# Kernel tuning notes

Hardware: AMD Instinct MI355X
Metric: run time of the kernel (lower is better)

The kernel has to match this reference:

```python
import jax, jax.numpy as jnp
import numpy as np

DIM = 768
NUM_HEADS = 12
POLY_DEG = 3
GRID = (24, 24)
BATCH = 16


def _make_powers():
    H, W = GRID
    ii, jj = np.meshgrid(np.arange(H), np.arange(W), indexing='ij')
    coords = np.stack([ii.ravel(), jj.ravel()], axis=-1).astype(np.float32)  # [HW, 2]
    dists = np.abs(coords[:, None, :] - coords[None, :, :]).sum(-1)  # L1 cdist [HW, HW]
    powers = np.stack([dists ** i for i in range(POLY_DEG + 1)], axis=0)  # [deg+1, HW, HW]
    return jnp.asarray(powers, dtype=jnp.float32)


def setup_inputs() -> dict:
    key = jax.random.key(0)
    ks = jax.random.split(key, 5)
    N = GRID[0] * GRID[1] + 1  # 577
    x = jax.random.normal(ks[0], (BATCH, N, DIM), dtype=jnp.float32)
    # nn.Linear weights stored as [in, out] for direct matmul; qkv_bias=False
    W_qkv = jax.random.normal(ks[1], (DIM, 3 * DIM), dtype=jnp.float32) * (DIM ** -0.5)
    W_proj = jax.random.normal(ks[2], (DIM, DIM), dtype=jnp.float32) * (DIM ** -0.5)
    b_proj = jnp.zeros((DIM,), dtype=jnp.float32)
    # small scale keeps polynomial bias (distances up to 46, cubed) numerically sane
    poly_coeffs = jax.random.normal(ks[3], (NUM_HEADS, POLY_DEG + 1), dtype=jnp.float32) * 0.01
    powers = _make_powers()
    return {"x": x, "W_qkv": W_qkv, "W_proj": W_proj, "b_proj": b_proj,
            "poly_coeffs": poly_coeffs, "powers": powers}


def reference(x, W_qkv, W_proj, b_proj, poly_coeffs, powers):
    B, N, C = x.shape
    h = NUM_HEADS
    d = C // h
    scale = d ** -0.5
    qkv = (x @ W_qkv).reshape(B, N, 3, h, d)
    qkv = jnp.transpose(qkv, (2, 0, 3, 1, 4))  # [3, B, h, N, d]
    q, k, v = qkv[0], qkv[1], qkv[2]
    # polynomial relative-position bias, padded with zeros for CLS row/col
    rpe = jnp.einsum('hd,dxy->hxy', poly_coeffs, powers)  # [h, HW, HW]
    rpe = jnp.pad(rpe, ((0, 0), (1, 0), (1, 0)))  # [h, N, N]
    attn = scale * jnp.einsum('bhnd,bhmd->bhnm', q, k) + rpe[None]
    attn = jax.nn.softmax(attn, axis=-1)
    out = jnp.einsum('bhnm,bhmd->bhnd', attn, v)
    out = jnp.transpose(out, (0, 2, 1, 3)).reshape(B, N, C)
    return out @ W_proj + b_proj
```

## Files before the change

### kernel.cpp

```cpp
#include <hip/hip_runtime.h>


using u16 = unsigned short;
using u32 = unsigned int;

typedef __bf16 bf16x8 __attribute__((ext_vector_type(8)));
typedef float f32x4 __attribute__((ext_vector_type(4)));

__device__ inline u16 f2bf(float f) {
    u32 u = __builtin_bit_cast(u32, f);
    u32 r = u + 0x7fffu + ((u >> 16) & 1u);
    return (u16)(r >> 16);
}
__device__ inline float bf2f(u16 x) {
    return __builtin_bit_cast(float, (u32)x << 16);
}

__device__ inline f32x4 mfma16(bf16x8 a, bf16x8 b, f32x4 c) {
    return __builtin_amdgcn_mfma_f32_16x16x32_bf16(a, b, c, 0, 0, 0);
}

__device__ inline float fexp2(float x) { return __builtin_amdgcn_exp2f(x); }

__device__ inline int xcd_remap(int bid, int nwg) {
    const int q = nwg >> 3, r = nwg & 7;
    const int xcd = bid & 7, idx = bid >> 3;
    return (xcd < r ? xcd * (q + 1) : r * (q + 1) + (xcd - r) * q) + idx;
}

__device__ inline float dpp_max16(float v) {
    int x;
    x = __builtin_amdgcn_update_dpp(0, __builtin_bit_cast(int, v), 0xB1, 0xF, 0xF, true);
    v = fmaxf(v, __builtin_bit_cast(float, x));
    x = __builtin_amdgcn_update_dpp(0, __builtin_bit_cast(int, v), 0x4E, 0xF, 0xF, true);
    v = fmaxf(v, __builtin_bit_cast(float, x));
    x = __builtin_amdgcn_update_dpp(0, __builtin_bit_cast(int, v), 0x124, 0xF, 0xF, true);
    v = fmaxf(v, __builtin_bit_cast(float, x));
    x = __builtin_amdgcn_update_dpp(0, __builtin_bit_cast(int, v), 0x128, 0xF, 0xF, true);
    v = fmaxf(v, __builtin_bit_cast(float, x));
    return v;
}
__device__ inline float dpp_sum16(float v) {
    int x;
    x = __builtin_amdgcn_update_dpp(0, __builtin_bit_cast(int, v), 0xB1, 0xF, 0xF, true);
    v += __builtin_bit_cast(float, x);
    x = __builtin_amdgcn_update_dpp(0, __builtin_bit_cast(int, v), 0x4E, 0xF, 0xF, true);
    v += __builtin_bit_cast(float, x);
    x = __builtin_amdgcn_update_dpp(0, __builtin_bit_cast(int, v), 0x124, 0xF, 0xF, true);
    v += __builtin_bit_cast(float, x);
    x = __builtin_amdgcn_update_dpp(0, __builtin_bit_cast(int, v), 0x128, 0xF, 0xF, true);
    v += __builtin_bit_cast(float, x);
    return v;
}

#define GLOAD_LDS16(g, l)                                                          \
    __builtin_amdgcn_global_load_lds((const __attribute__((address_space(1))) u32*)(g), \
                                     (__attribute__((address_space(3))) u32*)(l), 16, 0, 0)

#define BAR()    asm volatile("s_barrier" ::: "memory")
#define WAITV8() asm volatile("s_waitcnt vmcnt(8)" ::: "memory")
#define WAITV4() asm volatile("s_waitcnt vmcnt(4)" ::: "memory")
#define WAITV0() asm volatile("s_waitcnt vmcnt(0)" ::: "memory")

__global__ void k_prep(const float* __restrict__ x, const float* __restrict__ Wq,
                       const float* __restrict__ Wp, u16* __restrict__ xb,
                       u16* __restrict__ wqkv, u16* __restrict__ wprj) {
    const int bid = blockIdx.x;
    const int t = threadIdx.x;
    if (bid < 576) {
        __shared__ float tile[64][65];
        const float* src;
        u16* dst;
        int C, rt, ct;
        if (bid < 432) { src = Wq; dst = wqkv; C = 2304; rt = bid / 36; ct = bid % 36; }
        else { const int b2 = bid - 432; src = Wp; dst = wprj; C = 768; rt = b2 / 12; ct = b2 % 12; }
        const int row0 = rt * 64, col0 = ct * 64;
#pragma unroll
        for (int it = 0; it < 4; ++it) {
            const int row = it * 16 + (t >> 4);
            const float4 v = *(const float4*)&src[(size_t)(row0 + row) * C + col0 + (t & 15) * 4];
            tile[row][(t & 15) * 4 + 0] = v.x;
            tile[row][(t & 15) * 4 + 1] = v.y;
            tile[row][(t & 15) * 4 + 2] = v.z;
            tile[row][(t & 15) * 4 + 3] = v.w;
        }
        __syncthreads();
#pragma unroll
        for (int it = 0; it < 4; ++it) {
            const int oc = it * 16 + (t >> 4);
            const int orr = (t & 15) * 4;
            ushort4 o;
            o.x = f2bf(tile[orr + 0][oc]);
            o.y = f2bf(tile[orr + 1][oc]);
            o.z = f2bf(tile[orr + 2][oc]);
            o.w = f2bf(tile[orr + 3][oc]);
            *(ushort4*)&dst[(size_t)(col0 + oc) * 768 + row0 + orr] = o;
        }
    } else {
        const int n4 = 9232 * 768 / 4;
        const int stride = (2048 - 576) * 256;
        for (int i = (bid - 576) * 256 + t; i < n4; i += stride) {
            float4 v = ((const float4*)x)[i];
            ushort4 o;
            o.x = f2bf(v.x); o.y = f2bf(v.y); o.z = f2bf(v.z); o.w = f2bf(v.w);
            ((ushort4*)xb)[i] = o;
        }
    }
}

__device__ inline void stageAB(const u16* __restrict__ Ag, const u16* __restrict__ Bg,
                               u16* L, int t) {
#pragma unroll
    for (int c = 0; c < 2; ++c) {
        const int p = c * 256 + t;
        const int row = p >> 2, ch = p & 3;
        const int src = row * 768 + ((ch ^ ((row >> 1) & 3)) * 8);
        GLOAD_LDS16(Ag + src, L + p * 8);
        GLOAD_LDS16(Bg + src, L + 4096 + p * 8);
    }
}
__device__ inline bf16x8 ldfrag32(const u16* base, int row, int slot) {
    return *(const bf16x8*)(base + row * 32 + ((slot ^ ((row >> 1) & 3)) * 8));
}

template <int MODE, int NB>
__launch_bounds__(256, 2)
__global__ void k_gemm(const u16* __restrict__ A, const u16* __restrict__ Bw,
                       u16* __restrict__ q_out, u16* __restrict__ k_out,
                       u16* __restrict__ v_out,
                       float* __restrict__ f_out, const float* __restrict__ bias) {
    constexpr int NT = 24;
    constexpr int M = 9232;
    const int wgid = xcd_remap(blockIdx.x, gridDim.x);
    const int mbase = (wgid / NB) * 128;
    const int nbase = (wgid - (wgid / NB) * NB) * 128;
    __shared__ alignas(16) u16 lds[4][8192];
    const int t = threadIdx.x;
    const int lane = t & 63, w = t >> 6;
    const int lr = lane & 15, lg = lane >> 4;
    const int wrow = (w >> 1) * 64, wcol = (w & 1) * 64;
    const u16* Ag = A + (size_t)mbase * 768;
    const u16* Bg = Bw + (size_t)nbase * 768;
    f32x4 acc[4][4] = {};

    stageAB(Ag, Bg, &lds[0][0], t);
    stageAB(Ag + 32, Bg + 32, &lds[1][0], t);
    stageAB(Ag + 64, Bg + 64, &lds[2][0], t);
    WAITV8();
    BAR();

    for (int kt = 0; kt < NT; ++kt) {
        const u16* Lc = &lds[kt & 3][0];
        if (kt + 3 < NT)
            stageAB(Ag + (kt + 3) * 32, Bg + (kt + 3) * 32, &lds[(kt + 3) & 3][0], t);
        bf16x8 af[4], bv[4];
#pragma unroll
        for (int i = 0; i < 4; ++i)
            af[i] = ldfrag32(Lc, wrow + i * 16 + lr, lg);
#pragma unroll
        for (int j = 0; j < 4; ++j)
            bv[j] = ldfrag32(Lc + 4096, wcol + j * 16 + lr, lg);
        __builtin_amdgcn_s_setprio(1);
#pragma unroll
        for (int i = 0; i < 4; ++i)
#pragma unroll
            for (int j = 0; j < 4; ++j)
                acc[i][j] = mfma16(af[i], bv[j], acc[i][j]);
        __builtin_amdgcn_s_setprio(0);
        if (kt + 1 < NT) {
            if (kt < NT - 3)       { WAITV8(); }
            else if (kt == NT - 3) { WAITV4(); }
            else                   { WAITV0(); }
            BAR();
        }
    }

#pragma unroll
    for (int i = 0; i < 4; ++i) {
#pragma unroll
        for (int j = 0; j < 4; ++j) {
            const int col = nbase + wcol + j * 16 + lr;
#pragma unroll
            for (int r = 0; r < 4; ++r) {
                const int row = mbase + wrow + i * 16 + 4 * lg + r;
                if (row < M) {
                    if (MODE == 0) {
                        const int bb = row / 577;
                        const int nn = row - bb * 577;
                        const int tt = col / 768;
                        const int rem = col - tt * 768;
                        const int hh = rem >> 6, dd = rem & 63;
                        const size_t bh = (size_t)bb * 12 + hh;
                        const u16 val = f2bf(acc[i][j][r]);
                        if (tt == 0)      q_out[(bh * 640 + nn) * 64 + dd] = val;
                        else if (tt == 1) k_out[(bh * 640 + nn) * 64 + dd] = val;
                        else              v_out[(bh * 64 + dd) * 640 + nn] = val;
                    } else {
                        f_out[(size_t)row * 768 + col] = acc[i][j][r] + bias[col];
                    }
                }
            }
        }
    }
}

__launch_bounds__(256, 4)
__global__ void k_attn(const u16* __restrict__ Qg, const u16* __restrict__ Kg,
                       const u16* __restrict__ Vtg, const float* __restrict__ coef,
                       u16* __restrict__ Og) {
    const int wgid = xcd_remap(blockIdx.x, gridDim.x);
    const int bh = wgid / 9;
    const int qt = wgid - bh * 9;
    const int b = bh / 12, h = bh - b * 12;
    const int t = threadIdx.x;
    const int lane = t & 63, w = t >> 6;
    const int lr = lane & 15, lg = lane >> 4;
    __shared__ alignas(16) u16 Kl[2][4096];
    __shared__ alignas(16) u16 Vl[2][4096];
    __shared__ float lut[48];

    {
        const float l2e = 1.4426950408889634f;
        const float c0 = coef[h * 4 + 0] * l2e, c1 = coef[h * 4 + 1] * l2e,
                    c2 = coef[h * 4 + 2] * l2e, c3 = coef[h * 4 + 3] * l2e;
        if (t < 48) {
            const float d = (float)t;
            lut[t] = (t <= 46) ? (((c3 * d + c2) * d + c1) * d + c0) : 0.f;
        }
    }

    const int qrow0 = qt * 64 + w * 16;
    const u16* qp = Qg + ((size_t)bh * 640 + qrow0 + lr) * 64;
    const bf16x8 qa0 = *(const bf16x8*)(qp + lg * 8);
    const bf16x8 qa1 = *(const bf16x8*)(qp + 32 + lg * 8);

    float gi[4], gj[4];
#pragma unroll
    for (int r = 0; r < 4; ++r) {
        const int n = qrow0 + 4 * lg + r;
        if (n == 0) { gi[r] = 100.f; gj[r] = 0.f; }
        else {
            const int nm1 = n - 1;
            const int qi = nm1 / 24;
            gi[r] = (float)qi;
            gj[r] = (float)(nm1 - qi * 24);
        }
    }

    float M[4], L[4];
#pragma unroll
    for (int r = 0; r < 4; ++r) { M[r] = -3e38f; L[r] = 0.f; }
    f32x4 acco[4] = {};
    const float scale2 = 0.125f * 1.4426950408889634f;
    const int ch0 = ((lg ^ (lr & 7))) * 8;

    const u16* Ksb = Kg + (size_t)bh * 640 * 64;
    const u16* Vsb = Vtg + (size_t)bh * 64 * 640;
    const int pr0 = t >> 3, pc0 = t & 7;
    const int pr1 = (256 + t) >> 3, pc1 = (256 + t) & 7;
    const int kd0 = pr0 * 64 + ((pc0 ^ (pr0 & 7)) * 8);
    const int kd1 = pr1 * 64 + ((pc1 ^ (pr1 & 7)) * 8);
    const int vr0 = 16 * w + (lane >> 3), vc = lane & 7;
    const int vr1 = vr0 + 8;
    const int vd0 = vr0 * 64 + ((vc ^ (vr0 & 7)) * 8);
    const int vd1 = vr1 * 64 + ((vc ^ (vr1 & 7)) * 8);

    {
        uint4 k0 = *(const uint4*)(Ksb + pr0 * 64 + pc0 * 8);
        uint4 k1 = *(const uint4*)(Ksb + pr1 * 64 + pc1 * 8);
        uint4 v0 = *(const uint4*)(Vsb + (size_t)vr0 * 640 + vc * 8);
        uint4 v1 = *(const uint4*)(Vsb + (size_t)vr1 * 640 + vc * 8);
        *(uint4*)(&Kl[0][kd0]) = k0;
        *(uint4*)(&Kl[0][kd1]) = k1;
        *(uint4*)(&Vl[0][vd0]) = v0;
        *(uint4*)(&Vl[0][vd1]) = v1;
    }
    __syncthreads();
    int cur = 0;

    for (int kt = 0; kt < 9; ++kt) {
        const u16* Ks = Ksb + (size_t)(kt + 1) * 64 * 64;
        const u16* Vs = Vsb + (size_t)(kt + 1) * 64;
        const uint4 nk0 = *(const uint4*)(Ks + pr0 * 64 + pc0 * 8);
        const uint4 nk1 = *(const uint4*)(Ks + pr1 * 64 + pc1 * 8);
        const uint4 nv0 = *(const uint4*)(Vs + (size_t)vr0 * 640 + vc * 8);
        const uint4 nv1 = *(const uint4*)(Vs + (size_t)vr1 * 640 + vc * 8);

        const u16* Kc = &Kl[cur][0];
        const u16* Vc = &Vl[cur][0];
        u16* pw = &Vl[cur ^ 1][w * 1024];

        f32x4 sac[4];
        __builtin_amdgcn_s_setprio(1);
#pragma unroll
        for (int cb = 0; cb < 4; ++cb) {
            const int row = cb * 16 + lr;
            const bf16x8 kb0 = *(const bf16x8*)(Kc + row * 64 + ch0);
            const bf16x8 kb1 = *(const bf16x8*)(Kc + row * 64 + (ch0 ^ 32));
            f32x4 z = {};
            z = mfma16(qa0, kb0, z);
            sac[cb] = mfma16(qa1, kb1, z);
        }
        __builtin_amdgcn_s_setprio(0);

        float s[4][4], tm[4];
#pragma unroll
        for (int r = 0; r < 4; ++r) tm[r] = -3e38f;
#pragma unroll
        for (int cb = 0; cb < 4; ++cb) {
            const int m = kt * 64 + cb * 16 + lr;
            float ci, cj;
            if (m == 0) { ci = 200.f; cj = 0.f; }
            else {
                const int mm1 = m - 1;
                const int pi = mm1 / 24;
                ci = (float)pi;
                cj = (float)(mm1 - pi * 24);
            }
#pragma unroll
            for (int r = 0; r < 4; ++r) {
                const float df = fabsf(gi[r] - ci) + fabsf(gj[r] - cj);
                const int idx = min((int)df, 47);
                const float v = fmaf(sac[cb][r], scale2, lut[idx]);
                s[cb][r] = v;
                tm[r] = fmaxf(tm[r], v);
            }
        }
#pragma unroll
        for (int r = 0; r < 4; ++r) tm[r] = dpp_max16(tm[r]);

        float over = tm[0] - M[0];
        over = fmaxf(over, tm[1] - M[1]);
        over = fmaxf(over, tm[2] - M[2]);
        over = fmaxf(over, tm[3] - M[3]);
        if (__any(over > 11.5f)) {
#pragma unroll
            for (int r = 0; r < 4; ++r) {
                const float Mn = fmaxf(M[r], tm[r]);
                const float a = fexp2(M[r] - Mn);
                L[r] *= a;
                acco[0][r] *= a; acco[1][r] *= a;
                acco[2][r] *= a; acco[3][r] *= a;
                M[r] = Mn;
            }
        }

#pragma unroll
        for (int cb = 0; cb < 4; ++cb)
#pragma unroll
            for (int r = 0; r < 4; ++r) {
                const float p = fexp2(s[cb][r] - M[r]);
                L[r] += p;
                const int rw = 4 * lg + r;
                pw[rw * 64 + (((2 * cb + (lr >> 3)) ^ (rw & 7)) * 8) + (lr & 7)] = f2bf(p);
            }
        const bf16x8 pa0 = *(const bf16x8*)(pw + lr * 64 + ch0);
        const bf16x8 pa1 = *(const bf16x8*)(pw + lr * 64 + (ch0 ^ 32));
        __builtin_amdgcn_s_setprio(1);
#pragma unroll
        for (int f = 0; f < 4; ++f) {
            const int vrow = f * 16 + lr;
            const bf16x8 vb0 = *(const bf16x8*)(Vc + vrow * 64 + ch0);
            const bf16x8 vb1 = *(const bf16x8*)(Vc + vrow * 64 + (ch0 ^ 32));
            acco[f] = mfma16(pa0, vb0, acco[f]);
            acco[f] = mfma16(pa1, vb1, acco[f]);
        }
        __builtin_amdgcn_s_setprio(0);

        *(uint4*)(&Kl[cur ^ 1][kd0]) = nk0;
        *(uint4*)(&Kl[cur ^ 1][kd1]) = nk1;
        *(uint4*)(&Vl[cur ^ 1][vd0]) = nv0;
        *(uint4*)(&Vl[cur ^ 1][vd1]) = nv1;
        __syncthreads();
        cur ^= 1;
    }

    {
        const u16* Kc = &Kl[cur][0];
        const u16* Vc = &Vl[cur][0];
        u16* pw = &Vl[cur ^ 1][w * 1024];
        const bf16x8 kb0 = *(const bf16x8*)(Kc + lr * 64 + ch0);
        const bf16x8 kb1 = *(const bf16x8*)(Kc + lr * 64 + (ch0 ^ 32));
        f32x4 z = {};
        z = mfma16(qa0, kb0, z);
        const f32x4 sac0 = mfma16(qa1, kb1, z);

        float s0[4], tm[4];
#pragma unroll
        for (int r = 0; r < 4; ++r) {
            const float df = fabsf(gi[r] - 23.f) + fabsf(gj[r] - 23.f);
            float v = fmaf(sac0[r], scale2, lut[min((int)df, 47)]);
            v = (lr == 0) ? v : -1e30f;
            s0[r] = v;
            tm[r] = dpp_max16(v);
        }
        float over = tm[0] - M[0];
        over = fmaxf(over, tm[1] - M[1]);
        over = fmaxf(over, tm[2] - M[2]);
        over = fmaxf(over, tm[3] - M[3]);
        if (__any(over > 11.5f)) {
#pragma unroll
            for (int r = 0; r < 4; ++r) {
                const float Mn = fmaxf(M[r], tm[r]);
                const float a = fexp2(M[r] - Mn);
                L[r] *= a;
                acco[0][r] *= a; acco[1][r] *= a;
                acco[2][r] *= a; acco[3][r] *= a;
                M[r] = Mn;
            }
        }
#pragma unroll
        for (int cb = 0; cb < 4; ++cb)
#pragma unroll
            for (int r = 0; r < 4; ++r) {
                const float p = (cb == 0) ? fexp2(s0[r] - M[r]) : 0.f;
                L[r] += p;
                const int rw = 4 * lg + r;
                pw[rw * 64 + (((2 * cb + (lr >> 3)) ^ (rw & 7)) * 8) + (lr & 7)] = f2bf(p);
            }
        const bf16x8 pa0 = *(const bf16x8*)(pw + lr * 64 + ch0);
#pragma unroll
        for (int f = 0; f < 4; ++f) {
            const int vrow = f * 16 + lr;
            const bf16x8 vb0 = *(const bf16x8*)(Vc + vrow * 64 + ch0);
            acco[f] = mfma16(pa0, vb0, acco[f]);
        }
    }

    float inv[4];
#pragma unroll
    for (int r = 0; r < 4; ++r) inv[r] = __builtin_amdgcn_rcpf(dpp_sum16(L[r]));
#pragma unroll
    for (int f = 0; f < 4; ++f)
#pragma unroll
        for (int r = 0; r < 4; ++r) {
            const int n = qrow0 + 4 * lg + r;
            Og[((size_t)b * 577 + n) * 768 + h * 64 + f * 16 + lr] =
                f2bf(acco[f][r] * inv[r]);
        }
}

__launch_bounds__(256)
__global__ void k_attn_last(const u16* __restrict__ Qg, const u16* __restrict__ Kg,
                            const u16* __restrict__ Vtg, const float* __restrict__ coef,
                            u16* __restrict__ Og) {
    const int bh = blockIdx.x;
    const int b = bh / 12, h = bh - b * 12;
    const int t = threadIdx.x;
    const int lane = t & 63, w = t >> 6;
    __shared__ float qs[64];
    __shared__ float ps[640];
    __shared__ float red[4];
    __shared__ float opart[4][64];
    const float l2e = 1.4426950408889634f;
    const float c0 = coef[h * 4 + 0] * l2e, c1 = coef[h * 4 + 1] * l2e,
                c2 = coef[h * 4 + 2] * l2e, c3 = coef[h * 4 + 3] * l2e;
    const float scale2 = 0.125f * l2e;

    if (t < 64) qs[t] = bf2f(Qg[((size_t)bh * 640 + 576) * 64 + t]);
    __syncthreads();

    float sv[3];
#pragma unroll
    for (int u = 0; u < 3; ++u) {
        const int k = t + u * 256;
        float s = -3e38f;
        if (k < 577) {
            const u16* kp = Kg + ((size_t)bh * 640 + k) * 64;
            float acc = 0.f;
            for (int j = 0; j < 64; ++j) acc += qs[j] * bf2f(kp[j]);
            float rv = 0.f;
            if (k >= 1) {
                const int km1 = k - 1;
                const int ki = km1 / 24;
                const float d = fabsf(23.f - (float)ki) + fabsf(23.f - (float)(km1 - ki * 24));
                rv = ((c3 * d + c2) * d + c1) * d + c0;
            }
            s = fmaf(acc, scale2, rv);
        }
        sv[u] = s;
    }
    float v = fmaxf(fmaxf(sv[0], sv[1]), sv[2]);
    v = fmaxf(v, __shfl_xor(v, 1));  v = fmaxf(v, __shfl_xor(v, 2));
    v = fmaxf(v, __shfl_xor(v, 4));  v = fmaxf(v, __shfl_xor(v, 8));
    v = fmaxf(v, __shfl_xor(v, 16)); v = fmaxf(v, __shfl_xor(v, 32));
    if (lane == 0) red[w] = v;
    __syncthreads();
    const float Mx = fmaxf(fmaxf(red[0], red[1]), fmaxf(red[2], red[3]));

    float lsum = 0.f;
#pragma unroll
    for (int u = 0; u < 3; ++u) {
        const int k = t + u * 256;
        const float p = (k < 577) ? fexp2(sv[u] - Mx) : 0.f;
        if (k < 640) ps[k] = p;
        lsum += p;
    }
    lsum += __shfl_xor(lsum, 1);  lsum += __shfl_xor(lsum, 2);
    lsum += __shfl_xor(lsum, 4);  lsum += __shfl_xor(lsum, 8);
    lsum += __shfl_xor(lsum, 16); lsum += __shfl_xor(lsum, 32);
    __syncthreads();
    if (lane == 0) red[w] = lsum;
    __syncthreads();
    const float Lx = red[0] + red[1] + red[2] + red[3];

    const int d = t & 63, qd = t >> 6;
    const u16* vp = Vtg + ((size_t)bh * 64 + d) * 640;
    float o = 0.f;
    for (int k = qd * 160; k < qd * 160 + 160; ++k) o += ps[k] * bf2f(vp[k]);
    opart[qd][d] = o;
    __syncthreads();
    if (t < 64) {
        const float oo = (opart[0][t] + opart[1][t] + opart[2][t] + opart[3][t]) / Lx;
        Og[((size_t)b * 577 + 576) * 768 + h * 64 + t] = f2bf(oo);
    }
}

extern "C" void kernel_launch(void* const* d_in, const int* in_sizes, int n_in,
                              void* d_out, int out_size, void* d_ws, size_t ws_size,
                              hipStream_t stream) {
    const float* x      = (const float*)d_in[0];
    const float* W_qkv  = (const float*)d_in[1];
    const float* W_proj = (const float*)d_in[2];
    const float* b_proj = (const float*)d_in[3];
    const float* coef   = (const float*)d_in[4];
    float* out = (float*)d_out;
    char* ws = (char*)d_ws;

    u16* xb   = (u16*)(ws + 0);
    u16* Og   = (u16*)(ws + 0);
    u16* wqkv = (u16*)(ws + 14180352);
    u16* wprj = (u16*)(ws + 17719296);
    u16* Qg   = (u16*)(ws + 18898944);
    u16* Kg   = (u16*)(ws + 34627584);
    u16* Vtg  = (u16*)(ws + 50356224);

    k_prep<<<2048, 256, 0, stream>>>(x, W_qkv, W_proj, xb, wqkv, wprj);

    k_gemm<0, 18><<<18 * 73, 256, 0, stream>>>(xb, wqkv, Qg, Kg, Vtg,
                                               nullptr, nullptr);
    k_attn<<<1728, 256, 0, stream>>>(Qg, Kg, Vtg, coef, Og);
    k_attn_last<<<192, 256, 0, stream>>>(Qg, Kg, Vtg, coef, Og);
    k_gemm<1, 6><<<6 * 73, 256, 0, stream>>>(Og, wprj, nullptr, nullptr,
                                             nullptr, out, b_proj);
}
```

Before: 171.9 us.

## Load GEMM fragments directly from global memory instead of LDS pipeline

Removes the 4-stage LDS staging buffer, the async global-to-LDS copies and the per-iteration barriers from the GEMM kernel. Each wave now loads its MFMA operand fragments straight from global memory, and the occupancy hint rises to 4 blocks per CU now that no LDS is used. This drops barrier and LDS traffic overhead but loses operand sharing between waves, duplicating global and L2 reads. There is also no explicit prefetch, so load latency must be hidden by occupancy.

Result: slower. 285.6 us (+66.2%).

```diff
diff --git a/kernel.cpp b/kernel.cpp
--- a/kernel.cpp
+++ b/kernel.cpp
@@ -52,15 +52,6 @@
     v += __builtin_bit_cast(float, x);
     return v;
 }
-
-#define GLOAD_LDS16(g, l)                                                          \
-    __builtin_amdgcn_global_load_lds((const __attribute__((address_space(1))) u32*)(g), \
-                                     (__attribute__((address_space(3))) u32*)(l), 16, 0, 0)
-
-#define BAR()    asm volatile("s_barrier" ::: "memory")
-#define WAITV8() asm volatile("s_waitcnt vmcnt(8)" ::: "memory")
-#define WAITV4() asm volatile("s_waitcnt vmcnt(4)" ::: "memory")
-#define WAITV0() asm volatile("s_waitcnt vmcnt(0)" ::: "memory")
 
 __global__ void k_prep(const float* __restrict__ x, const float* __restrict__ Wq,
                        const float* __restrict__ Wp, u16* __restrict__ xb,
@@ -108,23 +99,8 @@
     }
 }
 
-__device__ inline void stageAB(const u16* __restrict__ Ag, const u16* __restrict__ Bg,
-                               u16* L, int t) {
-#pragma unroll
-    for (int c = 0; c < 2; ++c) {
-        const int p = c * 256 + t;
-        const int row = p >> 2, ch = p & 3;
-        const int src = row * 768 + ((ch ^ ((row >> 1) & 3)) * 8);
-        GLOAD_LDS16(Ag + src, L + p * 8);
-        GLOAD_LDS16(Bg + src, L + 4096 + p * 8);
-    }
-}
-__device__ inline bf16x8 ldfrag32(const u16* base, int row, int slot) {
-    return *(const bf16x8*)(base + row * 32 + ((slot ^ ((row >> 1) & 3)) * 8));
-}
-
 template <int MODE, int NB>
-__launch_bounds__(256, 2)
+__launch_bounds__(256, 4)
 __global__ void k_gemm(const u16* __restrict__ A, const u16* __restrict__ Bw,
                        u16* __restrict__ q_out, u16* __restrict__ k_out,
                        u16* __restrict__ v_out,
@@ -134,32 +110,24 @@
     const int wgid = xcd_remap(blockIdx.x, gridDim.x);
     const int mbase = (wgid / NB) * 128;
     const int nbase = (wgid - (wgid / NB) * NB) * 128;
-    __shared__ alignas(16) u16 lds[4][8192];
     const int t = threadIdx.x;
     const int lane = t & 63, w = t >> 6;
     const int lr = lane & 15, lg = lane >> 4;
     const int wrow = (w >> 1) * 64, wcol = (w & 1) * 64;
-    const u16* Ag = A + (size_t)mbase * 768;
-    const u16* Bg = Bw + (size_t)nbase * 768;
+    const u16* Ap = A + (size_t)(mbase + wrow + lr) * 768 + lg * 8;
+    const u16* Bp = Bw + (size_t)(nbase + wcol + lr) * 768 + lg * 8;
     f32x4 acc[4][4] = {};
 
-    stageAB(Ag, Bg, &lds[0][0], t);
-    stageAB(Ag + 32, Bg + 32, &lds[1][0], t);
-    stageAB(Ag + 64, Bg + 64, &lds[2][0], t);
-    WAITV8();
-    BAR();
-
+#pragma unroll 1
     for (int kt = 0; kt < NT; ++kt) {
-        const u16* Lc = &lds[kt & 3][0];
-        if (kt + 3 < NT)
-            stageAB(Ag + (kt + 3) * 32, Bg + (kt + 3) * 32, &lds[(kt + 3) & 3][0], t);
+        const int ko = kt * 32;
         bf16x8 af[4], bv[4];
 #pragma unroll
         for (int i = 0; i < 4; ++i)
-            af[i] = ldfrag32(Lc, wrow + i * 16 + lr, lg);
+            af[i] = *(const bf16x8*)(Ap + i * (16 * 768) + ko);
 #pragma unroll
         for (int j = 0; j < 4; ++j)
-            bv[j] = ldfrag32(Lc + 4096, wcol + j * 16 + lr, lg);
+            bv[j] = *(const bf16x8*)(Bp + j * (16 * 768) + ko);
         __builtin_amdgcn_s_setprio(1);
 #pragma unroll
         for (int i = 0; i < 4; ++i)
@@ -167,12 +135,6 @@
             for (int j = 0; j < 4; ++j)
                 acc[i][j] = mfma16(af[i], bv[j], acc[i][j]);
         __builtin_amdgcn_s_setprio(0);
-        if (kt + 1 < NT) {
-            if (kt < NT - 3)       { WAITV8(); }
-            else if (kt == NT - 3) { WAITV4(); }
-            else                   { WAITV0(); }
-            BAR();
-        }
     }
 
 #pragma unroll
```

## Process 32 query rows per wave and fold last-row kernel into attention

Applied to the files above, without the earlier changes.

Each wave now handles two 16-row query tiles (128 rows per block, 5 tiles per head), so every K/V tile loaded into LDS feeds twice as many MFMAs. The separate scalar k_attn_last kernel for row 576 is removed because the 640-row padded tiling now covers it, with a guard on the output store. The P staging buffers are moved into the idle halves of the K and V double buffers, and the next-tile global loads are issued later in the loop. Costs are roughly doubled accumulator and score registers, possible occupancy loss under launch_bounds(256,4), fewer blocks (960 instead of 1728), and wasted work on padded rows.

New measurement: 217.9 us. 1.27x slower.

```diff
diff --git a/kernel.cpp b/kernel.cpp
--- a/kernel.cpp
+++ b/kernel.cpp
@@ -209,8 +209,8 @@
                        const u16* __restrict__ Vtg, const float* __restrict__ coef,
                        u16* __restrict__ Og) {
     const int wgid = xcd_remap(blockIdx.x, gridDim.x);
-    const int bh = wgid / 9;
-    const int qt = wgid - bh * 9;
+    const int bh = wgid / 5;
+    const int qt = wgid - bh * 5;
     const int b = bh / 12, h = bh - b * 12;
     const int t = threadIdx.x;
     const int lane = t & 63, w = t >> 6;
@@ -229,83 +229,86 @@
         }
     }
 
-    const int qrow0 = qt * 64 + w * 16;
-    const u16* qp = Qg + ((size_t)bh * 640 + qrow0 + lr) * 64;
-    const bf16x8 qa0 = *(const bf16x8*)(qp + lg * 8);
-    const bf16x8 qa1 = *(const bf16x8*)(qp + 32 + lg * 8);
-
-    float gi[4], gj[4];
-#pragma unroll
-    for (int r = 0; r < 4; ++r) {
-        const int n = qrow0 + 4 * lg + r;
-        if (n == 0) { gi[r] = 100.f; gj[r] = 0.f; }
-        else {
-            const int nm1 = n - 1;
-            const int qi = nm1 / 24;
-            gi[r] = (float)qi;
-            gj[r] = (float)(nm1 - qi * 24);
-        }
-    }
-
-    float M[4], L[4];
-#pragma unroll
-    for (int r = 0; r < 4; ++r) { M[r] = -3e38f; L[r] = 0.f; }
-    f32x4 acco[4] = {};
+    const int qrow0 = qt * 128 + w * 32;
+    bf16x8 qa[2][2];
+#pragma unroll
+    for (int i = 0; i < 2; ++i) {
+        const u16* qp = Qg + ((size_t)bh * 640 + qrow0 + i * 16 + lr) * 64;
+        qa[i][0] = *(const bf16x8*)(qp + lg * 8);
+        qa[i][1] = *(const bf16x8*)(qp + 32 + lg * 8);
+    }
+
+    float gi[2][4], gj[2][4];
+#pragma unroll
+    for (int i = 0; i < 2; ++i)
+#pragma unroll
+        for (int r = 0; r < 4; ++r) {
+            const int n = qrow0 + i * 16 + 4 * lg + r;
+            if (n == 0) { gi[i][r] = 100.f; gj[i][r] = 0.f; }
+            else {
+                const int nm1 = n - 1;
+                const int qi = nm1 / 24;
+                gi[i][r] = (float)qi;
+                gj[i][r] = (float)(nm1 - qi * 24);
+            }
+        }
+
+    float M[2][4], L[2][4];
+#pragma unroll
+    for (int i = 0; i < 2; ++i)
+#pragma unroll
+        for (int r = 0; r < 4; ++r) { M[i][r] = -3e38f; L[i][r] = 0.f; }
+    f32x4 acco[2][4] = {};
     const float scale2 = 0.125f * 1.4426950408889634f;
     const int ch0 = ((lg ^ (lr & 7))) * 8;
 
     const u16* Ksb = Kg + (size_t)bh * 640 * 64;
     const u16* Vsb = Vtg + (size_t)bh * 64 * 640;
-    const int pr0 = t >> 3, pc0 = t & 7;
-    const int pr1 = (256 + t) >> 3, pc1 = (256 + t) & 7;
-    const int kd0 = pr0 * 64 + ((pc0 ^ (pr0 & 7)) * 8);
-    const int kd1 = pr1 * 64 + ((pc1 ^ (pr1 & 7)) * 8);
-    const int vr0 = 16 * w + (lane >> 3), vc = lane & 7;
-    const int vr1 = vr0 + 8;
-    const int vd0 = vr0 * 64 + ((vc ^ (vr0 & 7)) * 8);
-    const int vd1 = vr1 * 64 + ((vc ^ (vr1 & 7)) * 8);
+    const int sr0 = lane >> 3, sc = lane & 7;
+    const int kr0 = 16 * w + sr0, kr1 = kr0 + 8;
+    const int kd0 = kr0 * 64 + ((sc ^ (kr0 & 7)) * 8);
+    const int kd1 = kr1 * 64 + ((sc ^ (kr1 & 7)) * 8);
 
     {
-        uint4 k0 = *(const uint4*)(Ksb + pr0 * 64 + pc0 * 8);
-        uint4 k1 = *(const uint4*)(Ksb + pr1 * 64 + pc1 * 8);
-        uint4 v0 = *(const uint4*)(Vsb + (size_t)vr0 * 640 + vc * 8);
-        uint4 v1 = *(const uint4*)(Vsb + (size_t)vr1 * 640 + vc * 8);
+        uint4 k0 = *(const uint4*)(Ksb + kr0 * 64 + sc * 8);
+        uint4 k1 = *(const uint4*)(Ksb + kr1 * 64 + sc * 8);
+        uint4 v0 = *(const uint4*)(Vsb + (size_t)kr0 * 640 + sc * 8);
+        uint4 v1 = *(const uint4*)(Vsb + (size_t)kr1 * 640 + sc * 8);
         *(uint4*)(&Kl[0][kd0]) = k0;
         *(uint4*)(&Kl[0][kd1]) = k1;
-        *(uint4*)(&Vl[0][vd0]) = v0;
-        *(uint4*)(&Vl[0][vd1]) = v1;
+        *(uint4*)(&Vl[0][kd0]) = v0;
+        *(uint4*)(&Vl[0][kd1]) = v1;
     }
     __syncthreads();
     int cur = 0;
 
     for (int kt = 0; kt < 9; ++kt) {
-        const u16* Ks = Ksb + (size_t)(kt + 1) * 64 * 64;
-        const u16* Vs = Vsb + (size_t)(kt + 1) * 64;
-        const uint4 nk0 = *(const uint4*)(Ks + pr0 * 64 + pc0 * 8);
-        const uint4 nk1 = *(const uint4*)(Ks + pr1 * 64 + pc1 * 8);
-        const uint4 nv0 = *(const uint4*)(Vs + (size_t)vr0 * 640 + vc * 8);
-        const uint4 nv1 = *(const uint4*)(Vs + (size_t)vr1 * 640 + vc * 8);
-
         const u16* Kc = &Kl[cur][0];
         const u16* Vc = &Vl[cur][0];
-        u16* pw = &Vl[cur ^ 1][w * 1024];
-
-        f32x4 sac[4];
+        u16* pb0 = &Kl[cur ^ 1][16 * w * 64];
+        u16* pb1 = &Vl[cur ^ 1][16 * w * 64];
+
+        f32x4 sac[2][4];
         __builtin_amdgcn_s_setprio(1);
 #pragma unroll
         for (int cb = 0; cb < 4; ++cb) {
             const int row = cb * 16 + lr;
             const bf16x8 kb0 = *(const bf16x8*)(Kc + row * 64 + ch0);
             const bf16x8 kb1 = *(const bf16x8*)(Kc + row * 64 + (ch0 ^ 32));
-            f32x4 z = {};
-            z = mfma16(qa0, kb0, z);
-            sac[cb] = mfma16(qa1, kb1, z);
+#pragma unroll
+            for (int i = 0; i < 2; ++i) {
+                f32x4 z = {};
+                z = mfma16(qa[i][0], kb0, z);
+                sac[i][cb] = mfma16(qa[i][1], kb1, z);
+            }
         }
         __builtin_amdgcn_s_setprio(0);
 
-        float s[4][4], tm[4];
-#pragma unroll
-        for (int r = 0; r < 4; ++r) tm[r] = -3e38f;
+        float tm[2][4];
+#pragma unroll
+        for (int i = 0; i < 2; ++i)
+#pragma unroll
+            for (int r = 0; r < 4; ++r) tm[i][r] = -3e38f;
 #pragma unroll
         for (int cb = 0; cb < 4; ++cb) {
             const int m = kt * 64 + cb * 16 + lr;
@@ -318,59 +321,84 @@
                 cj = (float)(mm1 - pi * 24);
             }
 #pragma unroll
-            for (int r = 0; r < 4; ++r) {
-                const float df = fabsf(gi[r] - ci) + fabsf(gj[r] - cj);
-                const int idx = min((int)df, 47);
-                const float v = fmaf(sac[cb][r], scale2, lut[idx]);
-                s[cb][r] = v;
-                tm[r] = fmaxf(tm[r], v);
-            }
-        }
-#pragma unroll
-        for (int r = 0; r < 4; ++r) tm[r] = dpp_max16(tm[r]);
-
-        float over = tm[0] - M[0];
-        over = fmaxf(over, tm[1] - M[1]);
-        over = fmaxf(over, tm[2] - M[2]);
-        over = fmaxf(over, tm[3] - M[3]);
+            for (int i = 0; i < 2; ++i)
+#pragma unroll
+                for (int r = 0; r < 4; ++r) {
+                    const float df = fabsf(gi[i][r] - ci) + fabsf(gj[i][r] - cj);
+                    const float v = fmaf(sac[i][cb][r], scale2, lut[min((int)df, 47)]);
+                    sac[i][cb][r] = v;
+                    tm[i][r] = fmaxf(tm[i][r], v);
+                }
+        }
+#pragma unroll
+        for (int i = 0; i < 2; ++i)
+#pragma unroll
+            for (int r = 0; r < 4; ++r) tm[i][r] = dpp_max16(tm[i][r]);
+
+        float over = -3e38f;
+#pragma unroll
+        for (int i = 0; i < 2; ++i)
+#pragma unroll
+            for (int r = 0; r < 4; ++r) over = fmaxf(over, tm[i][r] - M[i][r]);
         if (__any(over > 11.5f)) {
 #pragma unroll
-            for (int r = 0; r < 4; ++r) {
-                const float Mn = fmaxf(M[r], tm[r]);
-                const float a = fexp2(M[r] - Mn);
-                L[r] *= a;
-                acco[0][r] *= a; acco[1][r] *= a;
-                acco[2][r] *= a; acco[3][r] *= a;
-                M[r] = Mn;
-            }
-        }
-
-#pragma unroll
-        for (int cb = 0; cb < 4; ++cb)
-#pragma unroll
-            for (int r = 0; r < 4; ++r) {
-                const float p = fexp2(s[cb][r] - M[r]);
-                L[r] += p;
-                const int rw = 4 * lg + r;
-                pw[rw * 64 + (((2 * cb + (lr >> 3)) ^ (rw & 7)) * 8) + (lr & 7)] = f2bf(p);
-            }
-        const bf16x8 pa0 = *(const bf16x8*)(pw + lr * 64 + ch0);
-        const bf16x8 pa1 = *(const bf16x8*)(pw + lr * 64 + (ch0 ^ 32));
+            for (int i = 0; i < 2; ++i)
+#pragma unroll
+                for (int r = 0; r < 4; ++r) {
+                    const float Mn = fmaxf(M[i][r], tm[i][r]);
+                    const float a = fexp2(M[i][r] - Mn);
+                    L[i][r] *= a;
+                    acco[i][0][r] *= a; acco[i][1][r] *= a;
+                    acco[i][2][r] *= a; acco[i][3][r] *= a;
+                    M[i][r] = Mn;
+                }
+        }
+
+#pragma unroll
+        for (int i = 0; i < 2; ++i) {
+            u16* pb = i ? pb1 : pb0;
+#pragma unroll
+            for (int cb = 0; cb < 4; ++cb)
+#pragma unroll
+                for (int r = 0; r < 4; ++r) {
+                    const float p = fexp2(sac[i][cb][r] - M[i][r]);
+                    L[i][r] += p;
+                    const int rw = 4 * lg + r;
+                    pb[rw * 64 + (((2 * cb + (lr >> 3)) ^ (rw & 7)) * 8) + (lr & 7)] = f2bf(p);
+                }
+        }
+
+        uint4 nk0, nk1, nv0, nv1;
+        {
+            const u16* Ks = Ksb + (size_t)(kt + 1) * 64 * 64;
+            const u16* Vs = Vsb + (size_t)(kt + 1) * 64;
+            nk0 = *(const uint4*)(Ks + kr0 * 64 + sc * 8);
+            nk1 = *(const uint4*)(Ks + kr1 * 64 + sc * 8);
+            nv0 = *(const uint4*)(Vs + (size_t)kr0 * 640 + sc * 8);
+            nv1 = *(const uint4*)(Vs + (size_t)kr1 * 640 + sc * 8);
+        }
+
+        const bf16x8 pa00 = *(const bf16x8*)(pb0 + lr * 64 + ch0);
+        const bf16x8 pa01 = *(const bf16x8*)(pb0 + lr * 64 + (ch0 ^ 32));
+        const bf16x8 pa10 = *(const bf16x8*)(pb1 + lr * 64 + ch0);
+        const bf16x8 pa11 = *(const bf16x8*)(pb1 + lr * 64 + (ch0 ^ 32));
         __builtin_amdgcn_s_setprio(1);
 #pragma unroll
         for (int f = 0; f < 4; ++f) {
             const int vrow = f * 16 + lr;
             const bf16x8 vb0 = *(const bf16x8*)(Vc + vrow * 64 + ch0);
             const bf16x8 vb1 = *(const bf16x8*)(Vc + vrow * 64 + (ch0 ^ 32));
-            acco[f] = mfma16(pa0, vb0, acco[f]);
-            acco[f] = mfma16(pa1, vb1, acco[f]);
+            acco[0][f] = mfma16(pa00, vb0, acco[0][f]);
+            acco[0][f] = mfma16(pa01, vb1, acco[0][f]);
+            acco[1][f] = mfma16(pa10, vb0, acco[1][f]);
+            acco[1][f] = mfma16(pa11, vb1, acco[1][f]);
         }
         __builtin_amdgcn_s_setprio(0);
 
         *(uint4*)(&Kl[cur ^ 1][kd0]) = nk0;
         *(uint4*)(&Kl[cur ^ 1][kd1]) = nk1;
-        *(uint4*)(&Vl[cur ^ 1][vd0]) = nv0;
-        *(uint4*)(&Vl[cur ^ 1][vd1]) = nv1;
+        *(uint4*)(&Vl[cur ^ 1][kd0]) = nv0;
+        *(uint4*)(&Vl[cur ^ 1][kd1]) = nv1;
         __syncthreads();
         cur ^= 1;
     }
@@ -378,142 +406,80 @@
     {
         const u16* Kc = &Kl[cur][0];
         const u16* Vc = &Vl[cur][0];
-        u16* pw = &Vl[cur ^ 1][w * 1024];
+        u16* pb0 = &Kl[cur ^ 1][16 * w * 64];
+        u16* pb1 = &Vl[cur ^ 1][16 * w * 64];
         const bf16x8 kb0 = *(const bf16x8*)(Kc + lr * 64 + ch0);
         const bf16x8 kb1 = *(const bf16x8*)(Kc + lr * 64 + (ch0 ^ 32));
-        f32x4 z = {};
-        z = mfma16(qa0, kb0, z);
-        const f32x4 sac0 = mfma16(qa1, kb1, z);
-
-        float s0[4], tm[4];
-#pragma unroll
-        for (int r = 0; r < 4; ++r) {
-            const float df = fabsf(gi[r] - 23.f) + fabsf(gj[r] - 23.f);
-            float v = fmaf(sac0[r], scale2, lut[min((int)df, 47)]);
-            v = (lr == 0) ? v : -1e30f;
-            s0[r] = v;
-            tm[r] = dpp_max16(v);
-        }
-        float over = tm[0] - M[0];
-        over = fmaxf(over, tm[1] - M[1]);
-        over = fmaxf(over, tm[2] - M[2]);
-        over = fmaxf(over, tm[3] - M[3]);
+        float s0[2][4], tm[2][4];
+#pragma unroll
+        for (int i = 0; i < 2; ++i) {
+            f32x4 z = {};
+            z = mfma16(qa[i][0], kb0, z);
+            const f32x4 sc0 = mfma16(qa[i][1], kb1, z);
+#pragma unroll
+            for (int r = 0; r < 4; ++r) {
+                const float df = fabsf(gi[i][r] - 23.f) + fabsf(gj[i][r] - 23.f);
+                float v = fmaf(sc0[r], scale2, lut[min((int)df, 47)]);
+                v = (lr == 0) ? v : -1e30f;
+                s0[i][r] = v;
+                tm[i][r] = dpp_max16(v);
+            }
+        }
+        float over = -3e38f;
+#pragma unroll
+        for (int i = 0; i < 2; ++i)
+#pragma unroll
+            for (int r = 0; r < 4; ++r) over = fmaxf(over, tm[i][r] - M[i][r]);
         if (__any(over > 11.5f)) {
 #pragma unroll
-            for (int r = 0; r < 4; ++r) {
-                const float Mn = fmaxf(M[r], tm[r]);
-                const float a = fexp2(M[r] - Mn);
-                L[r] *= a;
-                acco[0][r] *= a; acco[1][r] *= a;
-                acco[2][r] *= a; acco[3][r] *= a;
-                M[r] = Mn;
-            }
-        }
-#pragma unroll
-        for (int cb = 0; cb < 4; ++cb)
-#pragma unroll
-            for (int r = 0; r < 4; ++r) {
-                const float p = (cb == 0) ? fexp2(s0[r] - M[r]) : 0.f;
-                L[r] += p;
-                const int rw = 4 * lg + r;
-                pw[rw * 64 + (((2 * cb + (lr >> 3)) ^ (rw & 7)) * 8) + (lr & 7)] = f2bf(p);
-            }
-        const bf16x8 pa0 = *(const bf16x8*)(pw + lr * 64 + ch0);
+            for (int i = 0; i < 2; ++i)
+#pragma unroll
+                for (int r = 0; r < 4; ++r) {
+                    const float Mn = fmaxf(M[i][r], tm[i][r]);
+                    const float a = fexp2(M[i][r] - Mn);
+                    L[i][r] *= a;
+                    acco[i][0][r] *= a; acco[i][1][r] *= a;
+                    acco[i][2][r] *= a; acco[i][3][r] *= a;
+                    M[i][r] = Mn;
+                }
+        }
+#pragma unroll
+        for (int i = 0; i < 2; ++i) {
+            u16* pb = i ? pb1 : pb0;
+#pragma unroll
+            for (int cb = 0; cb < 4; ++cb)
+#pragma unroll
+                for (int r = 0; r < 4; ++r) {
+                    const float p = (cb == 0) ? fexp2(s0[i][r] - M[i][r]) : 0.f;
+                    L[i][r] += p;
+                    const int rw = 4 * lg + r;
+                    pb[rw * 64 + (((2 * cb + (lr >> 3)) ^ (rw & 7)) * 8) + (lr & 7)] = f2bf(p);
+                }
+        }
+        const bf16x8 pa00 = *(const bf16x8*)(pb0 + lr * 64 + ch0);
+        const bf16x8 pa10 = *(const bf16x8*)(pb1 + lr * 64 + ch0);
 #pragma unroll
         for (int f = 0; f < 4; ++f) {
             const int vrow = f * 16 + lr;
             const bf16x8 vb0 = *(const bf16x8*)(Vc + vrow * 64 + ch0);
-            acco[f] = mfma16(pa0, vb0, acco[f]);
-        }
-    }
-
-    float inv[4];
-#pragma unroll
-    for (int r = 0; r < 4; ++r) inv[r] = __builtin_amdgcn_rcpf(dpp_sum16(L[r]));
-#pragma unroll
-    for (int f = 0; f < 4; ++f)
+            acco[0][f] = mfma16(pa00, vb0, acco[0][f]);
+            acco[1][f] = mfma16(pa10, vb0, acco[1][f]);
+        }
+    }
+
+#pragma unroll
+    for (int i = 0; i < 2; ++i)
 #pragma unroll
         for (int r = 0; r < 4; ++r) {
-            const int n = qrow0 + 4 * lg + r;
-            Og[((size_t)b * 577 + n) * 768 + h * 64 + f * 16 + lr] =
-                f2bf(acco[f][r] * inv[r]);
-        }
-}
-
-__launch_bounds__(256)
-__global__ void k_attn_last(const u16* __restrict__ Qg, const u16* __restrict__ Kg,
-                            const u16* __restrict__ Vtg, const float* __restrict__ coef,
-                            u16* __restrict__ Og) {
-    const int bh = blockIdx.x;
-    const int b = bh / 12, h = bh - b * 12;
-    const int t = threadIdx.x;
-    const int lane = t & 63, w = t >> 6;
-    __shared__ float qs[64];
-    __shared__ float ps[640];
-    __shared__ float red[4];
-    __shared__ float opart[4][64];
-    const float l2e = 1.4426950408889634f;
-    const float c0 = coef[h * 4 + 0] * l2e, c1 = coef[h * 4 + 1] * l2e,
-                c2 = coef[h * 4 + 2] * l2e, c3 = coef[h * 4 + 3] * l2e;
-    const float scale2 = 0.125f * l2e;
-
-    if (t < 64) qs[t] = bf2f(Qg[((size_t)bh * 640 + 576) * 64 + t]);
-    __syncthreads();
-
-    float sv[3];
-#pragma unroll
-    for (int u = 0; u < 3; ++u) {
-        const int k = t + u * 256;
-        float s = -3e38f;
-        if (k < 577) {
-            const u16* kp = Kg + ((size_t)bh * 640 + k) * 64;
-            float acc = 0.f;
-            for (int j = 0; j < 64; ++j) acc += qs[j] * bf2f(kp[j]);
-            float rv = 0.f;
-            if (k >= 1) {
-                const int km1 = k - 1;
-                const int ki = km1 / 24;
-                const float d = fabsf(23.f - (float)ki) + fabsf(23.f - (float)(km1 - ki * 24));
-                rv = ((c3 * d + c2) * d + c1) * d + c0;
+            const float inv = __builtin_amdgcn_rcpf(dpp_sum16(L[i][r]));
+            const int n = qrow0 + i * 16 + 4 * lg + r;
+            if (n < 577) {
+#pragma unroll
+                for (int f = 0; f < 4; ++f)
+                    Og[((size_t)b * 577 + n) * 768 + h * 64 + f * 16 + lr] =
+                        f2bf(acco[i][f][r] * inv);
             }
-            s = fmaf(acc, scale2, rv);
-        }
-        sv[u] = s;
-    }
-    float v = fmaxf(fmaxf(sv[0], sv[1]), sv[2]);
-    v = fmaxf(v, __shfl_xor(v, 1));  v = fmaxf(v, __shfl_xor(v, 2));
-    v = fmaxf(v, __shfl_xor(v, 4));  v = fmaxf(v, __shfl_xor(v, 8));
-    v = fmaxf(v, __shfl_xor(v, 16)); v = fmaxf(v, __shfl_xor(v, 32));
-    if (lane == 0) red[w] = v;
-    __syncthreads();
-    const float Mx = fmaxf(fmaxf(red[0], red[1]), fmaxf(red[2], red[3]));
-
-    float lsum = 0.f;
-#pragma unroll
-    for (int u = 0; u < 3; ++u) {
-        const int k = t + u * 256;
-        const float p = (k < 577) ? fexp2(sv[u] - Mx) : 0.f;
-        if (k < 640) ps[k] = p;
-        lsum += p;
-    }
-    lsum += __shfl_xor(lsum, 1);  lsum += __shfl_xor(lsum, 2);
-    lsum += __shfl_xor(lsum, 4);  lsum += __shfl_xor(lsum, 8);
-    lsum += __shfl_xor(lsum, 16); lsum += __shfl_xor(lsum, 32);
-    __syncthreads();
-    if (lane == 0) red[w] = lsum;
-    __syncthreads();
-    const float Lx = red[0] + red[1] + red[2] + red[3];
-
-    const int d = t & 63, qd = t >> 6;
-    const u16* vp = Vtg + ((size_t)bh * 64 + d) * 640;
-    float o = 0.f;
-    for (int k = qd * 160; k < qd * 160 + 160; ++k) o += ps[k] * bf2f(vp[k]);
-    opart[qd][d] = o;
-    __syncthreads();
-    if (t < 64) {
-        const float oo = (opart[0][t] + opart[1][t] + opart[2][t] + opart[3][t]) / Lx;
-        Og[((size_t)b * 577 + 576) * 768 + h * 64 + t] = f2bf(oo);
-    }
+        }
 }
 
 extern "C" void kernel_launch(void* const* d_in, const int* in_sizes, int n_in,
@@ -539,8 +505,7 @@
 
     k_gemm<0, 18><<<18 * 73, 256, 0, stream>>>(xb, wqkv, Qg, Kg, Vtg,
                                                nullptr, nullptr);
-    k_attn<<<1728, 256, 0, stream>>>(Qg, Kg, Vtg, coef, Og);
-    k_attn_last<<<192, 256, 0, stream>>>(Qg, Kg, Vtg, coef, Og);
+    k_attn<<<960, 256, 0, stream>>>(Qg, Kg, Vtg, coef, Og);
     k_gemm<1, 6><<<6 * 73, 256, 0, stream>>>(Og, wprj, nullptr, nullptr,
                                              nullptr, out, b_proj);
 }
```
